# Kernel optimization log

Measured on AMD Instinct MI355X. Metric: run time of the kernel, lower is better.

The kernel has to match this reference:

```python
import jax, jax.numpy as jnp
import numpy as np

N_NODES = 50000
N_EDGES = 800000
D_IN = 64
D_OUT = 64


def setup_inputs() -> dict:
    key = jax.random.key(0)
    k = jax.random.split(key, 5)
    stdv = 1.0 / np.sqrt(D_OUT)
    X = jax.random.normal(k[0], (N_NODES, D_IN), jnp.float32)
    weights = jax.random.uniform(k[1], (D_IN, D_OUT), jnp.float32, -stdv, stdv)
    attention_w = jax.random.normal(k[2], (1, 1), jnp.float32)
    # edge list: row = destination (segment) ids, sorted (CSR-like); col = source ids
    row = jnp.sort(jax.random.randint(k[3], (N_EDGES,), 0, N_NODES, jnp.int32))
    col = jax.random.randint(k[4], (N_EDGES,), 0, N_NODES, jnp.int32)
    return {"X": X, "weights": weights, "attention_w": attention_w, "row": row, "col": col}


def reference(X, weights, attention_w, row, col):
    # dense linear
    Xp = X @ weights  # [N, D_OUT]
    # SDDMM: per-edge dot product between dst and src transformed features
    edge_feature = jnp.einsum('ed,ed->e', Xp[row], Xp[col])  # [E]
    # scale by scalar attention weight (n_heads = 1)
    edge_attn = edge_feature * attention_w[0, 0]  # [E]
    # SpMM aggregation: out[i] = sum_{e: row[e]=i} edge_attn[e] * Xp[col[e]]
    out = jax.ops.segment_sum(edge_attn[:, None] * Xp[col], row,
                              num_segments=X.shape[0])  # [N, D_OUT]
    return out
```

## Files before the change

kernel.cpp:

```cpp
#include <hip/hip_runtime.h>

#define D 64

__global__ __launch_bounds__(256) void gemm_kernel(const float* __restrict__ X,
                                                   const float* __restrict__ W,
                                                   float* __restrict__ Xp,
                                                   int nNodes) {
    int lane = threadIdx.x & 63;
    int wave = (blockIdx.x * 256 + threadIdx.x) >> 6;
    int nWaves = gridDim.x * 4;

    float w[D];
#pragma unroll
    for (int k = 0; k < D; ++k) w[k] = W[k * D + lane];

    for (int r = wave; r < nNodes; r += nWaves) {
        int row = __builtin_amdgcn_readfirstlane(r);
        const float4* xr = (const float4*)(X + (size_t)row * D);
        float acc = 0.f;
#pragma unroll
        for (int k4 = 0; k4 < D / 4; ++k4) {
            float4 xv = xr[k4];
            acc = fmaf(xv.x, w[4 * k4 + 0], acc);
            acc = fmaf(xv.y, w[4 * k4 + 1], acc);
            acc = fmaf(xv.z, w[4 * k4 + 2], acc);
            acc = fmaf(xv.w, w[4 * k4 + 3], acc);
        }
        Xp[(size_t)row * D + lane] = acc;
    }
}

__global__ __launch_bounds__(256) void rowptr_kernel(const int* __restrict__ row,
                                                     int* __restrict__ rowptr,
                                                     int nNodes, int nEdges) {
    int e = blockIdx.x * 256 + threadIdx.x;
    if (e >= nEdges) return;
    int r = row[e];
    int rprev = (e == 0) ? -1 : row[e - 1];
    for (int q = rprev + 1; q <= r; ++q) rowptr[q] = e;
    if (e == nEdges - 1) {
        for (int q = r + 1; q <= nNodes; ++q) rowptr[q] = nEdges;
    }
}

__global__ __launch_bounds__(256) void fused_kernel(const float* __restrict__ Xp,
                                                    const int* __restrict__ rowptr,
                                                    const int* __restrict__ col,
                                                    const float* __restrict__ attn_w,
                                                    float* __restrict__ out,
                                                    int nNodes) {
    int lane = threadIdx.x & 63;
    int node = (blockIdx.x * 256 + threadIdx.x) >> 6;
    if (node >= nNodes) return;
    int g = lane >> 4;
    int l = lane & 15;

    int eStart = rowptr[node];
    int eEnd   = rowptr[node + 1];
    float attn = attn_w[0];
    float4 xr = ((const float4*)(Xp + (size_t)node * D))[l];

    float4 acc0 = make_float4(0.f, 0.f, 0.f, 0.f);
    float4 acc1 = make_float4(0.f, 0.f, 0.f, 0.f);

    for (int base = eStart; base < eEnd; base += 8) {
        int e0 = base + g;
        int e1 = base + 4 + g;
        bool v0 = e0 < eEnd;
        bool v1 = e1 < eEnd;
        int c0 = col[v0 ? e0 : eStart];
        int c1 = col[v1 ? e1 : eStart];
        float4 x0 = ((const float4*)(Xp + (size_t)c0 * D))[l];
        float4 x1 = ((const float4*)(Xp + (size_t)c1 * D))[l];

        float p0 = x0.x * xr.x + x0.y * xr.y + x0.z * xr.z + x0.w * xr.w;
        float p1 = x1.x * xr.x + x1.y * xr.y + x1.z * xr.z + x1.w * xr.w;
#pragma unroll
        for (int off = 8; off > 0; off >>= 1) {
            p0 += __shfl_xor(p0, off, 64);
            p1 += __shfl_xor(p1, off, 64);
        }
        float s0 = v0 ? p0 * attn : 0.f;
        float s1 = v1 ? p1 * attn : 0.f;

        acc0.x = fmaf(s0, x0.x, acc0.x); acc0.y = fmaf(s0, x0.y, acc0.y);
        acc0.z = fmaf(s0, x0.z, acc0.z); acc0.w = fmaf(s0, x0.w, acc0.w);
        acc1.x = fmaf(s1, x1.x, acc1.x); acc1.y = fmaf(s1, x1.y, acc1.y);
        acc1.z = fmaf(s1, x1.z, acc1.z); acc1.w = fmaf(s1, x1.w, acc1.w);
    }

    acc0.x += acc1.x; acc0.y += acc1.y; acc0.z += acc1.z; acc0.w += acc1.w;
#pragma unroll
    for (int off = 16; off <= 32; off <<= 1) {
        acc0.x += __shfl_xor(acc0.x, off, 64);
        acc0.y += __shfl_xor(acc0.y, off, 64);
        acc0.z += __shfl_xor(acc0.z, off, 64);
        acc0.w += __shfl_xor(acc0.w, off, 64);
    }
    if (lane < 16) ((float4*)(out + (size_t)node * D))[lane] = acc0;
}

extern "C" void kernel_launch(void* const* d_in, const int* in_sizes, int n_in,
                              void* d_out, int out_size, void* d_ws, size_t ws_size,
                              hipStream_t stream) {
    const float* X    = (const float*)d_in[0];
    const float* W    = (const float*)d_in[1];
    const float* attn = (const float*)d_in[2];
    const int*   row  = (const int*)d_in[3];
    const int*   col  = (const int*)d_in[4];
    float* out = (float*)d_out;

    int nNodes = in_sizes[0] / D;
    int nEdges = in_sizes[3];

    float* Xp     = (float*)d_ws;
    int*   rowptr = (int*)(Xp + (size_t)nNodes * D);

    gemm_kernel<<<1024, 256, 0, stream>>>(X, W, Xp, nNodes);
    rowptr_kernel<<<(nEdges + 255) / 256, 256, 0, stream>>>(row, rowptr, nNodes, nEdges);
    fused_kernel<<<(nNodes + 3) / 4, 256, 0, stream>>>(Xp, rowptr, col, attn, out, nNodes);
}
```

Measured before the change: 120.0 us.

## Store transformed features in bf16 and batch column-index loads per wave

The intermediate Xp matrix is now written in bf16 instead of fp32, which halves the bytes moved by the random gathers in the fused SDDMM/SpMM kernel. Each lane now holds 8 features from a 16-byte load, so 8 edges are processed per wave step. Column indices are loaded 64 at a time with one coalesced read and broadcast with shuffles, replacing a per-step col load. The cost is reduced precision in the dot products and aggregation, which may exceed tolerance, plus the extra unpack work.

```diff
diff --git a/kernel.cpp b/kernel.cpp
--- a/kernel.cpp
+++ b/kernel.cpp
@@ -1,10 +1,23 @@
 #include <hip/hip_runtime.h>
+#include <hip/hip_bf16.h>
 
 #define D 64
 
+__device__ __forceinline__ void bf16x8_to_f32(uint4 u, float f[8]) {
+    union { unsigned int i; float x; } t;
+    t.i = u.x << 16;          f[0] = t.x;
+    t.i = u.x & 0xFFFF0000u;  f[1] = t.x;
+    t.i = u.y << 16;          f[2] = t.x;
+    t.i = u.y & 0xFFFF0000u;  f[3] = t.x;
+    t.i = u.z << 16;          f[4] = t.x;
+    t.i = u.z & 0xFFFF0000u;  f[5] = t.x;
+    t.i = u.w << 16;          f[6] = t.x;
+    t.i = u.w & 0xFFFF0000u;  f[7] = t.x;
+}
+
 __global__ __launch_bounds__(256) void gemm_kernel(const float* __restrict__ X,
                                                    const float* __restrict__ W,
-                                                   float* __restrict__ Xp,
+                                                   __hip_bfloat16* __restrict__ Xp,
                                                    int nNodes) {
     int lane = threadIdx.x & 63;
     int wave = (blockIdx.x * 256 + threadIdx.x) >> 6;
@@ -26,7 +39,7 @@
             acc = fmaf(xv.z, w[4 * k4 + 2], acc);
             acc = fmaf(xv.w, w[4 * k4 + 3], acc);
         }
-        Xp[(size_t)row * D + lane] = acc;
+        Xp[(size_t)row * D + lane] = __float2bfloat16(acc);
     }
 }
 
@@ -43,7 +56,7 @@
     }
 }
 
-__global__ __launch_bounds__(256) void fused_kernel(const float* __restrict__ Xp,
+__global__ __launch_bounds__(256) void fused_kernel(const __hip_bfloat16* __restrict__ Xp,
                                                     const int* __restrict__ rowptr,
                                                     const int* __restrict__ col,
                                                     const float* __restrict__ attn_w,
@@ -52,52 +65,61 @@
     int lane = threadIdx.x & 63;
     int node = (blockIdx.x * 256 + threadIdx.x) >> 6;
     if (node >= nNodes) return;
-    int g = lane >> 4;
-    int l = lane & 15;
+    int g = lane >> 3;
+    int j = lane & 7;
 
     int eStart = rowptr[node];
     int eEnd   = rowptr[node + 1];
     float attn = attn_w[0];
-    float4 xr = ((const float4*)(Xp + (size_t)node * D))[l];
 
-    float4 acc0 = make_float4(0.f, 0.f, 0.f, 0.f);
-    float4 acc1 = make_float4(0.f, 0.f, 0.f, 0.f);
+    const uint4* XpV = (const uint4*)Xp;
+    float xr[8];
+    bf16x8_to_f32(XpV[(size_t)node * 8 + j], xr);
 
-    for (int base = eStart; base < eEnd; base += 8) {
-        int e0 = base + g;
-        int e1 = base + 4 + g;
-        bool v0 = e0 < eEnd;
-        bool v1 = e1 < eEnd;
-        int c0 = col[v0 ? e0 : eStart];
-        int c1 = col[v1 ? e1 : eStart];
-        float4 x0 = ((const float4*)(Xp + (size_t)c0 * D))[l];
-        float4 x1 = ((const float4*)(Xp + (size_t)c1 * D))[l];
+    float acc[8] = {0.f, 0.f, 0.f, 0.f, 0.f, 0.f, 0.f, 0.f};
 
-        float p0 = x0.x * xr.x + x0.y * xr.y + x0.z * xr.z + x0.w * xr.w;
-        float p1 = x1.x * xr.x + x1.y * xr.y + x1.z * xr.z + x1.w * xr.w;
+    for (int cb = eStart; cb < eEnd; cb += 64) {
+        int myE = cb + lane;
+        int cidx = (myE < eEnd) ? col[myE] : -1;
+        int nrem = eEnd - cb;
+
 #pragma unroll
-        for (int off = 8; off > 0; off >>= 1) {
-            p0 += __shfl_xor(p0, off, 64);
-            p1 += __shfl_xor(p1, off, 64);
+        for (int m = 0; m < 4; ++m) {
+            if (16 * m >= nrem) break;
+            int c0 = __shfl(cidx, 16 * m + g, 64);
+            int c1 = __shfl(cidx, 16 * m + 8 + g, 64);
+            bool v0 = c0 >= 0, v1 = c1 >= 0;
+            uint4 u0 = XpV[(size_t)(v0 ? c0 : 0) * 8 + j];
+            uint4 u1 = XpV[(size_t)(v1 ? c1 : 0) * 8 + j];
+            float x0[8], x1[8];
+            bf16x8_to_f32(u0, x0);
+            bf16x8_to_f32(u1, x1);
+
+            float p0 = 0.f, p1 = 0.f;
+#pragma unroll
+            for (int q = 0; q < 8; ++q) { p0 = fmaf(xr[q], x0[q], p0);
+                                          p1 = fmaf(xr[q], x1[q], p1); }
+#pragma unroll
+            for (int off = 1; off < 8; off <<= 1) { p0 += __shfl_xor(p0, off, 64);
+                                                    p1 += __shfl_xor(p1, off, 64); }
+            float s0 = v0 ? p0 * attn : 0.f;
+            float s1 = v1 ? p1 * attn : 0.f;
+#pragma unroll
+            for (int q = 0; q < 8; ++q) { acc[q] = fmaf(s0, x0[q], acc[q]);
+                                          acc[q] = fmaf(s1, x1[q], acc[q]); }
         }
-        float s0 = v0 ? p0 * attn : 0.f;
-        float s1 = v1 ? p1 * attn : 0.f;
-
-        acc0.x = fmaf(s0, x0.x, acc0.x); acc0.y = fmaf(s0, x0.y, acc0.y);
-        acc0.z = fmaf(s0, x0.z, acc0.z); acc0.w = fmaf(s0, x0.w, acc0.w);
-        acc1.x = fmaf(s1, x1.x, acc1.x); acc1.y = fmaf(s1, x1.y, acc1.y);
-        acc1.z = fmaf(s1, x1.z, acc1.z); acc1.w = fmaf(s1, x1.w, acc1.w);
     }
 
-    acc0.x += acc1.x; acc0.y += acc1.y; acc0.z += acc1.z; acc0.w += acc1.w;
 #pragma unroll
-    for (int off = 16; off <= 32; off <<= 1) {
-        acc0.x += __shfl_xor(acc0.x, off, 64);
-        acc0.y += __shfl_xor(acc0.y, off, 64);
-        acc0.z += __shfl_xor(acc0.z, off, 64);
-        acc0.w += __shfl_xor(acc0.w, off, 64);
+    for (int off = 8; off < 64; off <<= 1)
+#pragma unroll
+        for (int q = 0; q < 8; ++q) acc[q] += __shfl_xor(acc[q], off, 64);
+
+    if (g == 0) {
+        float4* o = (float4*)(out + (size_t)node * D + 8 * j);
+        o[0] = make_float4(acc[0], acc[1], acc[2], acc[3]);
+        o[1] = make_float4(acc[4], acc[5], acc[6], acc[7]);
     }
-    if (lane < 16) ((float4*)(out + (size_t)node * D))[lane] = acc0;
 }
 
 extern "C" void kernel_launch(void* const* d_in, const int* in_sizes, int n_in,
@@ -113,8 +135,8 @@
     int nNodes = in_sizes[0] / D;
     int nEdges = in_sizes[3];
 
-    float* Xp     = (float*)d_ws;
-    int*   rowptr = (int*)(Xp + (size_t)nNodes * D);
+    __hip_bfloat16* Xp = (__hip_bfloat16*)d_ws;
+    int* rowptr = (int*)((char*)d_ws + (size_t)nNodes * D * sizeof(__hip_bfloat16));
 
     gemm_kernel<<<1024, 256, 0, stream>>>(X, W, Xp, nNodes);
     rowptr_kernel<<<(nEdges + 255) / 256, 256, 0, stream>>>(row, rowptr, nNodes, nEdges);
```

Measured after the change: 115.6 us. 3.7% less time.
